# Kernel optimization log

Measured on AMD Instinct MI355X. Metric: run time of the kernel, lower is better.

The kernel has to match this reference:

```python
import jax, jax.numpy as jnp
import numpy as np

N, E, D = 50000, 300000, 64
EPS = 0.0  # eps buffer, train_eps=False


def setup_inputs() -> dict:
    key = jax.random.key(0)
    ks = jax.random.split(key, 24)
    inp = {}
    i = 0
    for d in range(3):
        inp[f"x{d}"] = jax.random.normal(ks[i], (N, D), jnp.float32); i += 1
        inp[f"up_index{d}"] = jax.random.randint(ks[i], (2, E), 0, N, jnp.int32); i += 1
        inp[f"down_index{d}"] = jax.random.randint(ks[i], (2, E), 0, N, jnp.int32); i += 1
        inp[f"up_attr{d}"] = jax.random.normal(ks[i], (E, D), jnp.float32); i += 1
        inp[f"down_attr{d}"] = jax.random.normal(ks[i], (E, D), jnp.float32); i += 1
    s2 = 1.0 / np.sqrt(2 * D)
    s1 = 1.0 / np.sqrt(D)
    inp["W_up"] = jax.random.normal(ks[i], (2 * D, D), jnp.float32) * s2; i += 1
    inp["b_up"] = jnp.zeros((D,), jnp.float32)
    inp["W_down"] = jax.random.normal(ks[i], (2 * D, D), jnp.float32) * s2; i += 1
    inp["b_down"] = jnp.zeros((D,), jnp.float32)
    inp["W1"] = jax.random.normal(ks[i], (D, D), jnp.float32) * s1; i += 1
    inp["b1"] = jnp.zeros((D,), jnp.float32)
    inp["W2"] = jax.random.normal(ks[i], (D, D), jnp.float32) * s1; i += 1
    inp["b2"] = jnp.zeros((D,), jnp.float32)
    return inp


def _level(x, up_idx, down_idx, up_attr, down_attr,
           W_up, b_up, W_down, b_down, W1, b1, W2, b2):
    # message_up: gather source feats, concat attr, MLP, scatter-add to targets
    m_up = jax.nn.relu(jnp.concatenate([x[up_idx[1]], up_attr], axis=-1) @ W_up + b_up)
    out_up = jax.ops.segment_sum(m_up, up_idx[0], num_segments=N)
    m_dn = jax.nn.relu(jnp.concatenate([x[down_idx[1]], down_attr], axis=-1) @ W_down + b_down)
    out_dn = jax.ops.segment_sum(m_dn, down_idx[0], num_segments=N)
    # out_up += (1+eps)x; out_down += (1+eps)x; update(out_up + out_down)
    h = out_up + out_dn + (2.0 * (1.0 + EPS)) * x
    return jax.nn.relu(jax.nn.relu(h @ W1 + b1) @ W2 + b2)


def reference(x0, up_index0, down_index0, up_attr0, down_attr0,
              x1, up_index1, down_index1, up_attr1, down_attr1,
              x2, up_index2, down_index2, up_attr2, down_attr2,
              W_up, b_up, W_down, b_down, W1, b1, W2, b2):
    params = (W_up, b_up, W_down, b_down, W1, b1, W2, b2)
    o0 = _level(x0, up_index0, down_index0, up_attr0, down_attr0, *params)
    o1 = _level(x1, up_index1, down_index1, up_attr1, down_attr1, *params)
    o2 = _level(x2, up_index2, down_index2, up_attr2, down_attr2, *params)
    return (o0, o1, o2)
```

## Files before the change

kernel.cpp:

```cpp
#include <hip/hip_runtime.h>

#define NN 50000
#define NE 300000

typedef _Float16 f16;
typedef _Float16 f16x4 __attribute__((ext_vector_type(4)));
typedef float f32x4 __attribute__((ext_vector_type(4)));

#define A_STRIDE 136
#define A2_STRIDE 72

__device__ __forceinline__ f16x4 cvt4(float4 v) {
    f16x4 r; r.x = (f16)v.x; r.y = (f16)v.y; r.z = (f16)v.z; r.w = (f16)v.w;
    return r;
}

__global__ void init_kernel(const float* __restrict__ x, float* __restrict__ h, int n4) {
    int i = blockIdx.x * blockDim.x + threadIdx.x;
    if (i < n4) {
        float4 v = ((const float4*)x)[i];
        ((float4*)h)[i] = make_float4(2.f * v.x, 2.f * v.y, 2.f * v.z, 2.f * v.w);
    }
}

__global__ void edge_kernel(const float* __restrict__ x,
                            const int* __restrict__ tgt,
                            const int* __restrict__ src,
                            const float* __restrict__ attr,
                            const float* __restrict__ W,
                            const float* __restrict__ b,
                            float* __restrict__ h) {
    __shared__ f16 As[64 * A_STRIDE];
    __shared__ int tgt_s[64];
    __shared__ int src_s[64];

    const int t    = threadIdx.x;
    const int lane = t & 63;
    const int wid  = t >> 6;
    const int lr   = lane & 15;
    const int lg   = lane >> 4;

    f16x4 wf[8][4];
#pragma unroll
    for (int k0 = 0; k0 < 8; ++k0) {
        const int kb = k0 * 16 + 4 * lg;
#pragma unroll
        for (int n = 0; n < 4; ++n) {
            const int c = n * 16 + lr;
            f16x4 w;
            w.x = (f16)W[(kb + 0) * 64 + c];
            w.y = (f16)W[(kb + 1) * 64 + c];
            w.z = (f16)W[(kb + 2) * 64 + c];
            w.w = (f16)W[(kb + 3) * 64 + c];
            wf[k0][n] = w;
        }
    }
    float bf[4];
#pragma unroll
    for (int n = 0; n < 4; ++n) bf[n] = b[n * 16 + lr];

    const float4* x4 = (const float4*)x;
    const float4* a4 = (const float4*)attr;

    const int iters = (NE + 63) >> 6;
    for (int it = blockIdx.x; it < iters; it += gridDim.x) {
        const int e0 = it << 6;
        if (t < 64) {
            int e = e0 + t;
            tgt_s[t] = (e < NE) ? tgt[e] : -1;
            src_s[t] = (e < NE) ? src[e] : 0;
        }
        __syncthreads();

        {
            const int rb = t >> 4;
            const int cq = t & 15;
#pragma unroll
            for (int i = 0; i < 4; ++i) {
                const int rr = rb + i * 16;
                const int s  = src_s[rr];
                float4 vx = x4[s * 16 + cq];
                *(f16x4*)&As[rr * A_STRIDE + cq * 4] = cvt4(vx);
                const int e = e0 + rr;
                float4 va = (e < NE) ? a4[(size_t)e * 16 + cq]
                                     : make_float4(0.f, 0.f, 0.f, 0.f);
                *(f16x4*)&As[rr * A_STRIDE + 64 + cq * 4] = cvt4(va);
            }
        }
        __syncthreads();

        const int r0 = wid << 4;
        f32x4 acc[4];
#pragma unroll
        for (int n = 0; n < 4; ++n) acc[n] = (f32x4){0.f, 0.f, 0.f, 0.f};
#pragma unroll
        for (int k0 = 0; k0 < 8; ++k0) {
            f16x4 a = *(const f16x4*)&As[(r0 + lr) * A_STRIDE + k0 * 16 + 4 * lg];
#pragma unroll
            for (int n = 0; n < 4; ++n)
                acc[n] = __builtin_amdgcn_mfma_f32_16x16x16f16(a, wf[k0][n], acc[n], 0, 0, 0);
        }

#pragma unroll
        for (int n = 0; n < 4; ++n) {
#pragma unroll
            for (int j = 0; j < 4; ++j) {
                const int r  = 4 * lg + j;
                const int tg = tgt_s[r0 + r];
                float v = acc[n][j] + bf[n];
                v = v > 0.f ? v : 0.f;
                if (tg >= 0) unsafeAtomicAdd(&h[(size_t)tg * 64 + n * 16 + lr], v);
            }
        }
        __syncthreads();
    }
}

__global__ void node_kernel(float* __restrict__ io,
                            const float* __restrict__ W1, const float* __restrict__ b1,
                            const float* __restrict__ W2, const float* __restrict__ b2) {
    __shared__ f16 As[64 * A2_STRIDE];

    const int t    = threadIdx.x;
    const int lane = t & 63;
    const int wid  = t >> 6;
    const int lr   = lane & 15;
    const int lg   = lane >> 4;

    f16x4 w1f[4][4], w2f[4][4];
#pragma unroll
    for (int k0 = 0; k0 < 4; ++k0) {
        const int kb = k0 * 16 + 4 * lg;
#pragma unroll
        for (int n = 0; n < 4; ++n) {
            const int c = n * 16 + lr;
            f16x4 w;
            w.x = (f16)W1[(kb + 0) * 64 + c];
            w.y = (f16)W1[(kb + 1) * 64 + c];
            w.z = (f16)W1[(kb + 2) * 64 + c];
            w.w = (f16)W1[(kb + 3) * 64 + c];
            w1f[k0][n] = w;
            w.x = (f16)W2[(kb + 0) * 64 + c];
            w.y = (f16)W2[(kb + 1) * 64 + c];
            w.z = (f16)W2[(kb + 2) * 64 + c];
            w.w = (f16)W2[(kb + 3) * 64 + c];
            w2f[k0][n] = w;
        }
    }
    float b1f[4], b2f[4];
#pragma unroll
    for (int n = 0; n < 4; ++n) {
        b1f[n] = b1[n * 16 + lr];
        b2f[n] = b2[n * 16 + lr];
    }

    const float4* io4 = (const float4*)io;
    const int iters = (NN + 63) >> 6;
    for (int it = blockIdx.x; it < iters; it += gridDim.x) {
        const int n0 = it << 6;
        {
            const int rb = t >> 4;
            const int cq = t & 15;
#pragma unroll
            for (int i = 0; i < 4; ++i) {
                const int rr   = rb + i * 16;
                const int node = n0 + rr;
                float4 v = (node < NN) ? io4[(size_t)node * 16 + cq]
                                       : make_float4(0.f, 0.f, 0.f, 0.f);
                *(f16x4*)&As[rr * A2_STRIDE + cq * 4] = cvt4(v);
            }
        }
        __syncthreads();

        const int r0 = wid << 4;
        f32x4 acc[4];
#pragma unroll
        for (int n = 0; n < 4; ++n) acc[n] = (f32x4){0.f, 0.f, 0.f, 0.f};
#pragma unroll
        for (int k0 = 0; k0 < 4; ++k0) {
            f16x4 a = *(const f16x4*)&As[(r0 + lr) * A2_STRIDE + k0 * 16 + 4 * lg];
#pragma unroll
            for (int n = 0; n < 4; ++n)
                acc[n] = __builtin_amdgcn_mfma_f32_16x16x16f16(a, w1f[k0][n], acc[n], 0, 0, 0);
        }
#pragma unroll
        for (int n = 0; n < 4; ++n) {
#pragma unroll
            for (int j = 0; j < 4; ++j) {
                const int r = 4 * lg + j;
                float v = acc[n][j] + b1f[n];
                v = v > 0.f ? v : 0.f;
                As[(r0 + r) * A2_STRIDE + n * 16 + lr] = (f16)v;
            }
        }
        f32x4 acc2[4];
#pragma unroll
        for (int n = 0; n < 4; ++n) acc2[n] = (f32x4){0.f, 0.f, 0.f, 0.f};
#pragma unroll
        for (int k0 = 0; k0 < 4; ++k0) {
            f16x4 a = *(const f16x4*)&As[(r0 + lr) * A2_STRIDE + k0 * 16 + 4 * lg];
#pragma unroll
            for (int n = 0; n < 4; ++n)
                acc2[n] = __builtin_amdgcn_mfma_f32_16x16x16f16(a, w2f[k0][n], acc2[n], 0, 0, 0);
        }
#pragma unroll
        for (int n = 0; n < 4; ++n) {
#pragma unroll
            for (int j = 0; j < 4; ++j) {
                const int r    = 4 * lg + j;
                const int node = n0 + r0 + r;
                float v = acc2[n][j] + b2f[n];
                v = v > 0.f ? v : 0.f;
                if (node < NN) io[(size_t)node * 64 + n * 16 + lr] = v;
            }
        }
        __syncthreads();
    }
}

extern "C" void kernel_launch(void* const* d_in, const int* in_sizes, int n_in,
                              void* d_out, int out_size, void* d_ws, size_t ws_size,
                              hipStream_t stream) {
    (void)in_sizes; (void)n_in; (void)d_ws; (void)ws_size; (void)out_size;

    const float* W_up   = (const float*)d_in[15];
    const float* b_up   = (const float*)d_in[16];
    const float* W_down = (const float*)d_in[17];
    const float* b_down = (const float*)d_in[18];
    const float* W1     = (const float*)d_in[19];
    const float* b1     = (const float*)d_in[20];
    const float* W2     = (const float*)d_in[21];
    const float* b2     = (const float*)d_in[22];

    for (int d = 0; d < 3; ++d) {
        const float* x  = (const float*)d_in[5 * d + 0];
        const int*   ui = (const int*)  d_in[5 * d + 1];
        const int*   di = (const int*)  d_in[5 * d + 2];
        const float* ua = (const float*)d_in[5 * d + 3];
        const float* da = (const float*)d_in[5 * d + 4];
        float* h = (float*)d_out + (size_t)d * NN * 64;

        init_kernel<<<(NN * 16 + 255) / 256, 256, 0, stream>>>(x, h, NN * 16);
        edge_kernel<<<1024, 256, 0, stream>>>(x, ui, ui + NE, ua, W_up, b_up, h);
        edge_kernel<<<1024, 256, 0, stream>>>(x, di, di + NE, da, W_down, b_down, h);
        node_kernel<<<782, 256, 0, stream>>>(h, W1, b1, W2, b2);
    }
}
```

Measured before the change: 488.9 us.

## Batch all three levels into single init, edge and node launches

Merges the 12 per-level launches into three: one init kernel over all levels, one edge kernel covering all six edge sets via a job table indexed by blockIdx.y, and one node kernel for all three levels. The persistent grid-stride loops are replaced by one 64-row tile per block. This cuts launch overhead and the serialisation between small kernels, and gives each launch more parallel work. In exchange, each block now reloads its weight fragments into registers for a single tile, so weight-load cost is no longer amortised across many tiles.

```diff
diff --git a/kernel.cpp b/kernel.cpp
--- a/kernel.cpp
+++ b/kernel.cpp
@@ -2,6 +2,7 @@
 
 #define NN 50000
 #define NE 300000
+#define EDGE_TILES 4688
 
 typedef _Float16 f16;
 typedef _Float16 f16x4 __attribute__((ext_vector_type(4)));
@@ -10,29 +11,31 @@
 #define A_STRIDE 136
 #define A2_STRIDE 72
 
+struct Job { const float* x; const int* idx; const float* attr;
+             const float* W; const float* b; float* h; };
+struct Jobs6 { Job j[6]; };
+
 __device__ __forceinline__ f16x4 cvt4(float4 v) {
     f16x4 r; r.x = (f16)v.x; r.y = (f16)v.y; r.z = (f16)v.z; r.w = (f16)v.w;
     return r;
 }
 
-__global__ void init_kernel(const float* __restrict__ x, float* __restrict__ h, int n4) {
-    int i = blockIdx.x * blockDim.x + threadIdx.x;
-    if (i < n4) {
-        float4 v = ((const float4*)x)[i];
-        ((float4*)h)[i] = make_float4(2.f * v.x, 2.f * v.y, 2.f * v.z, 2.f * v.w);
-    }
-}
-
-__global__ void edge_kernel(const float* __restrict__ x,
-                            const int* __restrict__ tgt,
-                            const int* __restrict__ src,
-                            const float* __restrict__ attr,
-                            const float* __restrict__ W,
-                            const float* __restrict__ b,
-                            float* __restrict__ h) {
+__global__ void init_kernel(const float* __restrict__ x0, const float* __restrict__ x1,
+                            const float* __restrict__ x2, float* __restrict__ hbase) {
+    const float* xs[3] = {x0, x1, x2};
+    const int lvl = blockIdx.y;
+    const int i   = blockIdx.x * 256 + threadIdx.x;
+    float4 v = ((const float4*)xs[lvl])[i];
+    ((float4*)(hbase + (size_t)lvl * NN * 64))[i] =
+        make_float4(2.f * v.x, 2.f * v.y, 2.f * v.z, 2.f * v.w);
+}
+
+__global__ void edge_kernel(Jobs6 jobs) {
     __shared__ f16 As[64 * A_STRIDE];
     __shared__ int tgt_s[64];
     __shared__ int src_s[64];
+
+    const Job J = jobs.j[blockIdx.y];
 
     const int t    = threadIdx.x;
     const int lane = t & 63;
@@ -48,78 +51,75 @@
         for (int n = 0; n < 4; ++n) {
             const int c = n * 16 + lr;
             f16x4 w;
-            w.x = (f16)W[(kb + 0) * 64 + c];
-            w.y = (f16)W[(kb + 1) * 64 + c];
-            w.z = (f16)W[(kb + 2) * 64 + c];
-            w.w = (f16)W[(kb + 3) * 64 + c];
+            w.x = (f16)J.W[(kb + 0) * 64 + c];
+            w.y = (f16)J.W[(kb + 1) * 64 + c];
+            w.z = (f16)J.W[(kb + 2) * 64 + c];
+            w.w = (f16)J.W[(kb + 3) * 64 + c];
             wf[k0][n] = w;
         }
     }
     float bf[4];
 #pragma unroll
-    for (int n = 0; n < 4; ++n) bf[n] = b[n * 16 + lr];
-
-    const float4* x4 = (const float4*)x;
-    const float4* a4 = (const float4*)attr;
-
-    const int iters = (NE + 63) >> 6;
-    for (int it = blockIdx.x; it < iters; it += gridDim.x) {
-        const int e0 = it << 6;
-        if (t < 64) {
-            int e = e0 + t;
-            tgt_s[t] = (e < NE) ? tgt[e] : -1;
-            src_s[t] = (e < NE) ? src[e] : 0;
-        }
-        __syncthreads();
-
-        {
-            const int rb = t >> 4;
-            const int cq = t & 15;
-#pragma unroll
-            for (int i = 0; i < 4; ++i) {
-                const int rr = rb + i * 16;
-                const int s  = src_s[rr];
-                float4 vx = x4[s * 16 + cq];
-                *(f16x4*)&As[rr * A_STRIDE + cq * 4] = cvt4(vx);
-                const int e = e0 + rr;
-                float4 va = (e < NE) ? a4[(size_t)e * 16 + cq]
-                                     : make_float4(0.f, 0.f, 0.f, 0.f);
-                *(f16x4*)&As[rr * A_STRIDE + 64 + cq * 4] = cvt4(va);
-            }
-        }
-        __syncthreads();
-
-        const int r0 = wid << 4;
-        f32x4 acc[4];
-#pragma unroll
-        for (int n = 0; n < 4; ++n) acc[n] = (f32x4){0.f, 0.f, 0.f, 0.f};
-#pragma unroll
-        for (int k0 = 0; k0 < 8; ++k0) {
-            f16x4 a = *(const f16x4*)&As[(r0 + lr) * A_STRIDE + k0 * 16 + 4 * lg];
-#pragma unroll
-            for (int n = 0; n < 4; ++n)
-                acc[n] = __builtin_amdgcn_mfma_f32_16x16x16f16(a, wf[k0][n], acc[n], 0, 0, 0);
-        }
-
-#pragma unroll
-        for (int n = 0; n < 4; ++n) {
-#pragma unroll
-            for (int j = 0; j < 4; ++j) {
-                const int r  = 4 * lg + j;
-                const int tg = tgt_s[r0 + r];
-                float v = acc[n][j] + bf[n];
-                v = v > 0.f ? v : 0.f;
-                if (tg >= 0) unsafeAtomicAdd(&h[(size_t)tg * 64 + n * 16 + lr], v);
-            }
-        }
-        __syncthreads();
-    }
-}
-
-__global__ void node_kernel(float* __restrict__ io,
+    for (int n = 0; n < 4; ++n) bf[n] = J.b[n * 16 + lr];
+
+    const int e0 = blockIdx.x << 6;
+    if (t < 64) {
+        int e = e0 + t;
+        tgt_s[t] = (e < NE) ? J.idx[e] : -1;
+        src_s[t] = (e < NE) ? J.idx[NE + e] : 0;
+    }
+    __syncthreads();
+
+    {
+        const float4* x4 = (const float4*)J.x;
+        const float4* a4 = (const float4*)J.attr;
+        const int rb = t >> 4;
+        const int cq = t & 15;
+#pragma unroll
+        for (int i = 0; i < 4; ++i) {
+            const int rr = rb + i * 16;
+            const int s  = src_s[rr];
+            float4 vx = x4[(size_t)s * 16 + cq];
+            *(f16x4*)&As[rr * A_STRIDE + cq * 4] = cvt4(vx);
+            const int e = e0 + rr;
+            float4 va = (e < NE) ? a4[(size_t)e * 16 + cq]
+                                 : make_float4(0.f, 0.f, 0.f, 0.f);
+            *(f16x4*)&As[rr * A_STRIDE + 64 + cq * 4] = cvt4(va);
+        }
+    }
+    __syncthreads();
+
+    const int r0 = wid << 4;
+    f32x4 acc[4];
+#pragma unroll
+    for (int n = 0; n < 4; ++n) acc[n] = (f32x4){0.f, 0.f, 0.f, 0.f};
+#pragma unroll
+    for (int k0 = 0; k0 < 8; ++k0) {
+        f16x4 a = *(const f16x4*)&As[(r0 + lr) * A_STRIDE + k0 * 16 + 4 * lg];
+#pragma unroll
+        for (int n = 0; n < 4; ++n)
+            acc[n] = __builtin_amdgcn_mfma_f32_16x16x16f16(a, wf[k0][n], acc[n], 0, 0, 0);
+    }
+
+#pragma unroll
+    for (int n = 0; n < 4; ++n) {
+#pragma unroll
+        for (int j = 0; j < 4; ++j) {
+            const int r  = 4 * lg + j;
+            const int tg = tgt_s[r0 + r];
+            float v = acc[n][j] + bf[n];
+            v = v > 0.f ? v : 0.f;
+            if (tg >= 0) unsafeAtomicAdd(&J.h[(size_t)tg * 64 + n * 16 + lr], v);
+        }
+    }
+}
+
+__global__ void node_kernel(float* __restrict__ hbase,
                             const float* __restrict__ W1, const float* __restrict__ b1,
                             const float* __restrict__ W2, const float* __restrict__ b2) {
     __shared__ f16 As[64 * A2_STRIDE];
+
+    float* io = hbase + (size_t)blockIdx.y * NN * 64;
 
     const int t    = threadIdx.x;
     const int lane = t & 63;
@@ -155,66 +155,62 @@
     }
 
     const float4* io4 = (const float4*)io;
-    const int iters = (NN + 63) >> 6;
-    for (int it = blockIdx.x; it < iters; it += gridDim.x) {
-        const int n0 = it << 6;
-        {
-            const int rb = t >> 4;
-            const int cq = t & 15;
-#pragma unroll
-            for (int i = 0; i < 4; ++i) {
-                const int rr   = rb + i * 16;
-                const int node = n0 + rr;
-                float4 v = (node < NN) ? io4[(size_t)node * 16 + cq]
-                                       : make_float4(0.f, 0.f, 0.f, 0.f);
-                *(f16x4*)&As[rr * A2_STRIDE + cq * 4] = cvt4(v);
-            }
-        }
-        __syncthreads();
-
-        const int r0 = wid << 4;
-        f32x4 acc[4];
-#pragma unroll
-        for (int n = 0; n < 4; ++n) acc[n] = (f32x4){0.f, 0.f, 0.f, 0.f};
-#pragma unroll
-        for (int k0 = 0; k0 < 4; ++k0) {
-            f16x4 a = *(const f16x4*)&As[(r0 + lr) * A2_STRIDE + k0 * 16 + 4 * lg];
-#pragma unroll
-            for (int n = 0; n < 4; ++n)
-                acc[n] = __builtin_amdgcn_mfma_f32_16x16x16f16(a, w1f[k0][n], acc[n], 0, 0, 0);
-        }
-#pragma unroll
-        for (int n = 0; n < 4; ++n) {
-#pragma unroll
-            for (int j = 0; j < 4; ++j) {
-                const int r = 4 * lg + j;
-                float v = acc[n][j] + b1f[n];
-                v = v > 0.f ? v : 0.f;
-                As[(r0 + r) * A2_STRIDE + n * 16 + lr] = (f16)v;
-            }
-        }
-        f32x4 acc2[4];
-#pragma unroll
-        for (int n = 0; n < 4; ++n) acc2[n] = (f32x4){0.f, 0.f, 0.f, 0.f};
-#pragma unroll
-        for (int k0 = 0; k0 < 4; ++k0) {
-            f16x4 a = *(const f16x4*)&As[(r0 + lr) * A2_STRIDE + k0 * 16 + 4 * lg];
-#pragma unroll
-            for (int n = 0; n < 4; ++n)
-                acc2[n] = __builtin_amdgcn_mfma_f32_16x16x16f16(a, w2f[k0][n], acc2[n], 0, 0, 0);
-        }
-#pragma unroll
-        for (int n = 0; n < 4; ++n) {
-#pragma unroll
-            for (int j = 0; j < 4; ++j) {
-                const int r    = 4 * lg + j;
-                const int node = n0 + r0 + r;
-                float v = acc2[n][j] + b2f[n];
-                v = v > 0.f ? v : 0.f;
-                if (node < NN) io[(size_t)node * 64 + n * 16 + lr] = v;
-            }
-        }
-        __syncthreads();
+    const int n0 = blockIdx.x << 6;
+    {
+        const int rb = t >> 4;
+        const int cq = t & 15;
+#pragma unroll
+        for (int i = 0; i < 4; ++i) {
+            const int rr   = rb + i * 16;
+            const int node = n0 + rr;
+            float4 v = (node < NN) ? io4[(size_t)node * 16 + cq]
+                                   : make_float4(0.f, 0.f, 0.f, 0.f);
+            *(f16x4*)&As[rr * A2_STRIDE + cq * 4] = cvt4(v);
+        }
+    }
+    __syncthreads();
+
+    const int r0 = wid << 4;
+    f32x4 acc[4];
+#pragma unroll
+    for (int n = 0; n < 4; ++n) acc[n] = (f32x4){0.f, 0.f, 0.f, 0.f};
+#pragma unroll
+    for (int k0 = 0; k0 < 4; ++k0) {
+        f16x4 a = *(const f16x4*)&As[(r0 + lr) * A2_STRIDE + k0 * 16 + 4 * lg];
+#pragma unroll
+        for (int n = 0; n < 4; ++n)
+            acc[n] = __builtin_amdgcn_mfma_f32_16x16x16f16(a, w1f[k0][n], acc[n], 0, 0, 0);
+    }
+#pragma unroll
+    for (int n = 0; n < 4; ++n) {
+#pragma unroll
+        for (int j = 0; j < 4; ++j) {
+            const int r = 4 * lg + j;
+            float v = acc[n][j] + b1f[n];
+            v = v > 0.f ? v : 0.f;
+            As[(r0 + r) * A2_STRIDE + n * 16 + lr] = (f16)v;
+        }
+    }
+    f32x4 acc2[4];
+#pragma unroll
+    for (int n = 0; n < 4; ++n) acc2[n] = (f32x4){0.f, 0.f, 0.f, 0.f};
+#pragma unroll
+    for (int k0 = 0; k0 < 4; ++k0) {
+        f16x4 a = *(const f16x4*)&As[(r0 + lr) * A2_STRIDE + k0 * 16 + 4 * lg];
+#pragma unroll
+        for (int n = 0; n < 4; ++n)
+            acc2[n] = __builtin_amdgcn_mfma_f32_16x16x16f16(a, w2f[k0][n], acc2[n], 0, 0, 0);
+    }
+#pragma unroll
+    for (int n = 0; n < 4; ++n) {
+#pragma unroll
+        for (int j = 0; j < 4; ++j) {
+            const int r    = 4 * lg + j;
+            const int node = n0 + r0 + r;
+            float v = acc2[n][j] + b2f[n];
+            v = v > 0.f ? v : 0.f;
+            if (node < NN) io[(size_t)node * 64 + n * 16 + lr] = v;
+        }
     }
 }
 
@@ -232,17 +228,22 @@
     const float* W2     = (const float*)d_in[21];
     const float* b2     = (const float*)d_in[22];
 
+    float* hbase = (float*)d_out;
+
+    Jobs6 jobs;
     for (int d = 0; d < 3; ++d) {
         const float* x  = (const float*)d_in[5 * d + 0];
         const int*   ui = (const int*)  d_in[5 * d + 1];
         const int*   di = (const int*)  d_in[5 * d + 2];
         const float* ua = (const float*)d_in[5 * d + 3];
         const float* da = (const float*)d_in[5 * d + 4];
-        float* h = (float*)d_out + (size_t)d * NN * 64;
-
-        init_kernel<<<(NN * 16 + 255) / 256, 256, 0, stream>>>(x, h, NN * 16);
-        edge_kernel<<<1024, 256, 0, stream>>>(x, ui, ui + NE, ua, W_up, b_up, h);
-        edge_kernel<<<1024, 256, 0, stream>>>(x, di, di + NE, da, W_down, b_down, h);
-        node_kernel<<<782, 256, 0, stream>>>(h, W1, b1, W2, b2);
-    }
-}
+        float* h = hbase + (size_t)d * NN * 64;
+        jobs.j[2 * d + 0] = {x, ui, ua, W_up,   b_up,   h};
+        jobs.j[2 * d + 1] = {x, di, da, W_down, b_down, h};
+    }
+
+    init_kernel<<<dim3(3125, 3), 256, 0, stream>>>(
+        (const float*)d_in[0], (const float*)d_in[5], (const float*)d_in[10], hbase);
+    edge_kernel<<<dim3(EDGE_TILES, 6), 256, 0, stream>>>(jobs);
+    node_kernel<<<dim3(782, 3), 256, 0, stream>>>(hbase, W1, b1, W2, b2);
+}
```

Result: slower. 855.4 us (+75.0%).

## Accumulate edge messages in fp16 workspace with half2 atomics, per-wave tiles, batched launches

Applied to the files above, without the earlier changes.

Scatter-add accumulation moves from fp32 in the output buffer to an fp16 buffer in the workspace, using packed half2 atomics built from lane shuffles. This halves atomic traffic and the intermediate footprint. The edge kernel now works on 16-edge tiles per wave and gathers straight into registers, dropping shared-memory staging and block barriers. Init and node kernels each run once across all three levels, cutting launches. Accumulating in fp16 risks precision loss and overflow in the sums.

```diff
diff --git a/kernel.cpp b/kernel.cpp
--- a/kernel.cpp
+++ b/kernel.cpp
@@ -1,44 +1,50 @@
 #include <hip/hip_runtime.h>
+#include <hip/hip_fp16.h>
 
 #define NN 50000
 #define NE 300000
+#define ETILES (NE / 16)
+#define NTILES (NN / 16)
 
 typedef _Float16 f16;
 typedef _Float16 f16x4 __attribute__((ext_vector_type(4)));
 typedef float f32x4 __attribute__((ext_vector_type(4)));
 
-#define A_STRIDE 136
-#define A2_STRIDE 72
-
 __device__ __forceinline__ f16x4 cvt4(float4 v) {
     f16x4 r; r.x = (f16)v.x; r.y = (f16)v.y; r.z = (f16)v.z; r.w = (f16)v.w;
     return r;
 }
 
-__global__ void init_kernel(const float* __restrict__ x, float* __restrict__ h, int n4) {
-    int i = blockIdx.x * blockDim.x + threadIdx.x;
-    if (i < n4) {
-        float4 v = ((const float4*)x)[i];
-        ((float4*)h)[i] = make_float4(2.f * v.x, 2.f * v.y, 2.f * v.z, 2.f * v.w);
-    }
-}
-
-__global__ void edge_kernel(const float* __restrict__ x,
-                            const int* __restrict__ tgt,
-                            const int* __restrict__ src,
-                            const float* __restrict__ attr,
-                            const float* __restrict__ W,
-                            const float* __restrict__ b,
-                            float* __restrict__ h) {
-    __shared__ f16 As[64 * A_STRIDE];
-    __shared__ int tgt_s[64];
-    __shared__ int src_s[64];
+template<bool HALF>
+__global__ void init_kernel(const float* __restrict__ x0, const float* __restrict__ x1,
+                            const float* __restrict__ x2, void* __restrict__ hbase) {
+    const size_t i = (size_t)blockIdx.x * 256 + threadIdx.x;
+    const int lvl = (int)(i / (NN * 16));
+    const size_t li = i - (size_t)lvl * (NN * 16);
+    const float* xs = (lvl == 0) ? x0 : (lvl == 1) ? x1 : x2;
+    float4 v = ((const float4*)xs)[li];
+    if (HALF) {
+        f16x4 o;
+        o.x = (f16)(2.f * v.x); o.y = (f16)(2.f * v.y);
+        o.z = (f16)(2.f * v.z); o.w = (f16)(2.f * v.w);
+        ((f16x4*)((f16*)hbase + (size_t)lvl * NN * 64))[li] = o;
+    } else {
+        ((float4*)((float*)hbase + (size_t)lvl * NN * 64))[li] =
+            make_float4(2.f * v.x, 2.f * v.y, 2.f * v.z, 2.f * v.w);
+    }
+}
+
+template<bool HALF>
+__global__ __launch_bounds__(256) void edge_kernel(
+    const float* __restrict__ x, const int* __restrict__ idx,
+    const float* __restrict__ attr, const float* __restrict__ W,
+    const float* __restrict__ b, void* __restrict__ hv) {
 
     const int t    = threadIdx.x;
     const int lane = t & 63;
     const int wid  = t >> 6;
     const int lr   = lane & 15;
-    const int lg   = lane >> 4;
+    const int lg   = (lane >> 4) & 3;
 
     f16x4 wf[8][4];
 #pragma unroll
@@ -62,70 +68,72 @@
     const float4* x4 = (const float4*)x;
     const float4* a4 = (const float4*)attr;
 
-    const int iters = (NE + 63) >> 6;
-    for (int it = blockIdx.x; it < iters; it += gridDim.x) {
-        const int e0 = it << 6;
-        if (t < 64) {
-            int e = e0 + t;
-            tgt_s[t] = (e < NE) ? tgt[e] : -1;
-            src_s[t] = (e < NE) ? src[e] : 0;
-        }
-        __syncthreads();
-
-        {
-            const int rb = t >> 4;
-            const int cq = t & 15;
-#pragma unroll
-            for (int i = 0; i < 4; ++i) {
-                const int rr = rb + i * 16;
-                const int s  = src_s[rr];
-                float4 vx = x4[s * 16 + cq];
-                *(f16x4*)&As[rr * A_STRIDE + cq * 4] = cvt4(vx);
-                const int e = e0 + rr;
-                float4 va = (e < NE) ? a4[(size_t)e * 16 + cq]
-                                     : make_float4(0.f, 0.f, 0.f, 0.f);
-                *(f16x4*)&As[rr * A_STRIDE + 64 + cq * 4] = cvt4(va);
+    const int gw     = blockIdx.x * 4 + wid;
+    const int stride = gridDim.x * 4;
+    for (int tile = gw; tile < ETILES; tile += stride) {
+        const int e0  = tile << 4;
+        const int src = idx[NE + e0 + lr];
+        int tg[4];
+#pragma unroll
+        for (int j = 0; j < 4; ++j) tg[j] = idx[e0 + 4 * lg + j];
+
+        f16x4 a[8];
+#pragma unroll
+        for (int k0 = 0; k0 < 4; ++k0)
+            a[k0] = cvt4(x4[(size_t)src * 16 + 4 * k0 + lg]);
+#pragma unroll
+        for (int k0 = 0; k0 < 4; ++k0)
+            a[4 + k0] = cvt4(a4[(size_t)(e0 + lr) * 16 + 4 * k0 + lg]);
+
+        f32x4 acc[4];
+#pragma unroll
+        for (int n = 0; n < 4; ++n) acc[n] = (f32x4){0.f, 0.f, 0.f, 0.f};
+#pragma unroll
+        for (int k0 = 0; k0 < 8; ++k0) {
+#pragma unroll
+            for (int n = 0; n < 4; ++n)
+                acc[n] = __builtin_amdgcn_mfma_f32_16x16x16f16(a[k0], wf[k0][n], acc[n], 0, 0, 0);
+        }
+
+#pragma unroll
+        for (int j = 0; j < 4; ++j) {
+            float v[4], vn[4];
+#pragma unroll
+            for (int n = 0; n < 4; ++n) v[n] = fmaxf(acc[n][j] + bf[n], 0.f);
+#pragma unroll
+            for (int n = 0; n < 4; ++n) vn[n] = __shfl_xor(v[n], 1);
+            if (HALF) {
+                __half* hp = (__half*)hv + (size_t)tg[j] * 64;
+                if ((lane & 1) == 0) {
+                    unsafeAtomicAdd((__half2*)(hp + 0 * 16 + lr), __floats2half2_rn(v[0], vn[0]));
+                    unsafeAtomicAdd((__half2*)(hp + 1 * 16 + lr), __floats2half2_rn(v[1], vn[1]));
+                } else {
+                    unsafeAtomicAdd((__half2*)(hp + 2 * 16 + lr - 1), __floats2half2_rn(vn[2], v[2]));
+                    unsafeAtomicAdd((__half2*)(hp + 3 * 16 + lr - 1), __floats2half2_rn(vn[3], v[3]));
+                }
+            } else {
+                float* hp = (float*)hv + (size_t)tg[j] * 64;
+#pragma unroll
+                for (int n = 0; n < 4; ++n)
+                    unsafeAtomicAdd(hp + n * 16 + lr, v[n]);
             }
         }
-        __syncthreads();
-
-        const int r0 = wid << 4;
-        f32x4 acc[4];
-#pragma unroll
-        for (int n = 0; n < 4; ++n) acc[n] = (f32x4){0.f, 0.f, 0.f, 0.f};
-#pragma unroll
-        for (int k0 = 0; k0 < 8; ++k0) {
-            f16x4 a = *(const f16x4*)&As[(r0 + lr) * A_STRIDE + k0 * 16 + 4 * lg];
-#pragma unroll
-            for (int n = 0; n < 4; ++n)
-                acc[n] = __builtin_amdgcn_mfma_f32_16x16x16f16(a, wf[k0][n], acc[n], 0, 0, 0);
-        }
-
-#pragma unroll
-        for (int n = 0; n < 4; ++n) {
-#pragma unroll
-            for (int j = 0; j < 4; ++j) {
-                const int r  = 4 * lg + j;
-                const int tg = tgt_s[r0 + r];
-                float v = acc[n][j] + bf[n];
-                v = v > 0.f ? v : 0.f;
-                if (tg >= 0) unsafeAtomicAdd(&h[(size_t)tg * 64 + n * 16 + lr], v);
-            }
-        }
-        __syncthreads();
-    }
-}
-
-__global__ void node_kernel(float* __restrict__ io,
-                            const float* __restrict__ W1, const float* __restrict__ b1,
-                            const float* __restrict__ W2, const float* __restrict__ b2) {
-    __shared__ f16 As[64 * A2_STRIDE];
+    }
+}
+
+template<bool HALF>
+__global__ __launch_bounds__(256) void node_kernel(
+    const void* __restrict__ hbase, float* __restrict__ outb,
+    const float* __restrict__ W1, const float* __restrict__ b1,
+    const float* __restrict__ W2, const float* __restrict__ b2) {
+
+    __shared__ f16 Y[4][16 * 72];
 
     const int t    = threadIdx.x;
     const int lane = t & 63;
     const int wid  = t >> 6;
     const int lr   = lane & 15;
-    const int lg   = lane >> 4;
+    const int lg   = (lane >> 4) & 3;
 
     f16x4 w1f[4][4], w2f[4][4];
 #pragma unroll
@@ -154,74 +162,73 @@
         b2f[n] = b2[n * 16 + lr];
     }
 
-    const float4* io4 = (const float4*)io;
-    const int iters = (NN + 63) >> 6;
-    for (int it = blockIdx.x; it < iters; it += gridDim.x) {
-        const int n0 = it << 6;
-        {
-            const int rb = t >> 4;
-            const int cq = t & 15;
-#pragma unroll
-            for (int i = 0; i < 4; ++i) {
-                const int rr   = rb + i * 16;
-                const int node = n0 + rr;
-                float4 v = (node < NN) ? io4[(size_t)node * 16 + cq]
-                                       : make_float4(0.f, 0.f, 0.f, 0.f);
-                *(f16x4*)&As[rr * A2_STRIDE + cq * 4] = cvt4(v);
-            }
-        }
-        __syncthreads();
-
-        const int r0 = wid << 4;
+    const int gw     = blockIdx.x * 4 + wid;
+    const int stride = gridDim.x * 4;
+    for (int tile = gw; tile < 3 * NTILES; tile += stride) {
+        const int lvl = tile / NTILES;
+        const int n0  = (tile - lvl * NTILES) << 4;
+        float* out = outb + (size_t)lvl * NN * 64;
+
+        f16x4 a[4];
+        if (HALF) {
+            const f16* h16 = (const f16*)hbase + (size_t)lvl * NN * 64;
+#pragma unroll
+            for (int k0 = 0; k0 < 4; ++k0)
+                a[k0] = *(const f16x4*)&h16[(size_t)(n0 + lr) * 64 + k0 * 16 + 4 * lg];
+        } else {
+            const float4* h4 = (const float4*)((const float*)hbase + (size_t)lvl * NN * 64);
+#pragma unroll
+            for (int k0 = 0; k0 < 4; ++k0)
+                a[k0] = cvt4(h4[(size_t)(n0 + lr) * 16 + 4 * k0 + lg]);
+        }
+
         f32x4 acc[4];
 #pragma unroll
         for (int n = 0; n < 4; ++n) acc[n] = (f32x4){0.f, 0.f, 0.f, 0.f};
 #pragma unroll
-        for (int k0 = 0; k0 < 4; ++k0) {
-            f16x4 a = *(const f16x4*)&As[(r0 + lr) * A2_STRIDE + k0 * 16 + 4 * lg];
+        for (int k0 = 0; k0 < 4; ++k0)
 #pragma unroll
             for (int n = 0; n < 4; ++n)
-                acc[n] = __builtin_amdgcn_mfma_f32_16x16x16f16(a, w1f[k0][n], acc[n], 0, 0, 0);
-        }
-#pragma unroll
-        for (int n = 0; n < 4; ++n) {
+                acc[n] = __builtin_amdgcn_mfma_f32_16x16x16f16(a[k0], w1f[k0][n], acc[n], 0, 0, 0);
+
+#pragma unroll
+        for (int n = 0; n < 4; ++n)
 #pragma unroll
             for (int j = 0; j < 4; ++j) {
-                const int r = 4 * lg + j;
                 float v = acc[n][j] + b1f[n];
                 v = v > 0.f ? v : 0.f;
-                As[(r0 + r) * A2_STRIDE + n * 16 + lr] = (f16)v;
+                Y[wid][(4 * lg + j) * 72 + n * 16 + lr] = (f16)v;
             }
-        }
+
+        f16x4 a2[4];
+#pragma unroll
+        for (int k0 = 0; k0 < 4; ++k0)
+            a2[k0] = *(const f16x4*)&Y[wid][lr * 72 + k0 * 16 + 4 * lg];
+
         f32x4 acc2[4];
 #pragma unroll
         for (int n = 0; n < 4; ++n) acc2[n] = (f32x4){0.f, 0.f, 0.f, 0.f};
 #pragma unroll
-        for (int k0 = 0; k0 < 4; ++k0) {
-            f16x4 a = *(const f16x4*)&As[(r0 + lr) * A2_STRIDE + k0 * 16 + 4 * lg];
+        for (int k0 = 0; k0 < 4; ++k0)
 #pragma unroll
             for (int n = 0; n < 4; ++n)
-                acc2[n] = __builtin_amdgcn_mfma_f32_16x16x16f16(a, w2f[k0][n], acc2[n], 0, 0, 0);
-        }
-#pragma unroll
-        for (int n = 0; n < 4; ++n) {
+                acc2[n] = __builtin_amdgcn_mfma_f32_16x16x16f16(a2[k0], w2f[k0][n], acc2[n], 0, 0, 0);
+
+#pragma unroll
+        for (int n = 0; n < 4; ++n)
 #pragma unroll
             for (int j = 0; j < 4; ++j) {
-                const int r    = 4 * lg + j;
-                const int node = n0 + r0 + r;
                 float v = acc2[n][j] + b2f[n];
                 v = v > 0.f ? v : 0.f;
-                if (node < NN) io[(size_t)node * 64 + n * 16 + lr] = v;
+                out[(size_t)(n0 + 4 * lg + j) * 64 + n * 16 + lr] = v;
             }
-        }
-        __syncthreads();
     }
 }
 
 extern "C" void kernel_launch(void* const* d_in, const int* in_sizes, int n_in,
                               void* d_out, int out_size, void* d_ws, size_t ws_size,
                               hipStream_t stream) {
-    (void)in_sizes; (void)n_in; (void)d_ws; (void)ws_size; (void)out_size;
+    (void)in_sizes; (void)n_in; (void)out_size;
 
     const float* W_up   = (const float*)d_in[15];
     const float* b_up   = (const float*)d_in[16];
@@ -232,17 +239,39 @@
     const float* W2     = (const float*)d_in[21];
     const float* b2     = (const float*)d_in[22];
 
-    for (int d = 0; d < 3; ++d) {
-        const float* x  = (const float*)d_in[5 * d + 0];
-        const int*   ui = (const int*)  d_in[5 * d + 1];
-        const int*   di = (const int*)  d_in[5 * d + 2];
-        const float* ua = (const float*)d_in[5 * d + 3];
-        const float* da = (const float*)d_in[5 * d + 4];
-        float* h = (float*)d_out + (size_t)d * NN * 64;
-
-        init_kernel<<<(NN * 16 + 255) / 256, 256, 0, stream>>>(x, h, NN * 16);
-        edge_kernel<<<1024, 256, 0, stream>>>(x, ui, ui + NE, ua, W_up, b_up, h);
-        edge_kernel<<<1024, 256, 0, stream>>>(x, di, di + NE, da, W_down, b_down, h);
-        node_kernel<<<782, 256, 0, stream>>>(h, W1, b1, W2, b2);
-    }
-}
+    const float* x0 = (const float*)d_in[0];
+    const float* x1 = (const float*)d_in[5];
+    const float* x2 = (const float*)d_in[10];
+
+    const bool half_ok = ws_size >= (size_t)3 * NN * 64 * sizeof(__half);
+
+    if (half_ok) {
+        f16* hbase = (f16*)d_ws;
+        init_kernel<true><<<9375, 256, 0, stream>>>(x0, x1, x2, hbase);
+        for (int d = 0; d < 3; ++d) {
+            const float* x  = (const float*)d_in[5 * d + 0];
+            const int*   ui = (const int*)  d_in[5 * d + 1];
+            const int*   di = (const int*)  d_in[5 * d + 2];
+            const float* ua = (const float*)d_in[5 * d + 3];
+            const float* da = (const float*)d_in[5 * d + 4];
+            void* h = hbase + (size_t)d * NN * 64;
+            edge_kernel<true><<<1024, 256, 0, stream>>>(x, ui, ua, W_up,   b_up,   h);
+            edge_kernel<true><<<1024, 256, 0, stream>>>(x, di, da, W_down, b_down, h);
+        }
+        node_kernel<true><<<586, 256, 0, stream>>>(hbase, (float*)d_out, W1, b1, W2, b2);
+    } else {
+        float* hbase = (float*)d_out;
+        init_kernel<false><<<9375, 256, 0, stream>>>(x0, x1, x2, hbase);
+        for (int d = 0; d < 3; ++d) {
+            const float* x  = (const float*)d_in[5 * d + 0];
+            const int*   ui = (const int*)  d_in[5 * d + 1];
+            const int*   di = (const int*)  d_in[5 * d + 2];
+            const float* ua = (const float*)d_in[5 * d + 3];
+            const float* da = (const float*)d_in[5 * d + 4];
+            void* h = hbase + (size_t)d * NN * 64;
+            edge_kernel<false><<<1024, 256, 0, stream>>>(x, ui, ua, W_up,   b_up,   h);
+            edge_kernel<false><<<1024, 256, 0, stream>>>(x, di, da, W_down, b_down, h);
+        }
+        node_kernel<false><<<586, 256, 0, stream>>>(hbase, (float*)d_out, W1, b1, W2, b2);
+    }
+}
```

New measurement: 468.8 us. -4.1%, faster.
